# Kernel optimization log

Hardware: AMD Instinct MI355X
Metric: run time of the kernel (lower is better)

Reference implementation:

```python
import jax, jax.numpy as jnp
import numpy as np


def grid_sample_3d(vol, grid):
    """torch F.grid_sample 3D, mode='bilinear' (trilinear), align_corners=True.
    vol:  [B, C, Din, Hin, Win]
    grid: [B, Dout, Hout, Wout, 3] with xyz in [-1, 1] (x->W, y->H, z->D)
    returns [B, C, Dout, Hout, Wout]
    """
    B, C, Din, Hin, Win = vol.shape
    v = jnp.transpose(vol, (0, 2, 3, 4, 1))
    # align_corners=True: -1 -> 0, +1 -> size-1
    ix = (grid[..., 0] + 1.0) * 0.5 * (Win - 1)
    iy = (grid[..., 1] + 1.0) * 0.5 * (Hin - 1)
    iz = (grid[..., 2] + 1.0) * 0.5 * (Din - 1)
    x0 = jnp.floor(ix); y0 = jnp.floor(iy); z0 = jnp.floor(iz)
    wx = (ix - x0)[..., None]
    wy = (iy - y0)[..., None]
    wz = (iz - z0)[..., None]
    x0i = jnp.clip(x0.astype(jnp.int32), 0, Win - 1); x1i = jnp.clip(x0i + 1, 0, Win - 1)
    y0i = jnp.clip(y0.astype(jnp.int32), 0, Hin - 1); y1i = jnp.clip(y0i + 1, 0, Hin - 1)
    z0i = jnp.clip(z0.astype(jnp.int32), 0, Din - 1); z1i = jnp.clip(z0i + 1, 0, Din - 1)
    b = jnp.arange(B)[:, None, None, None]
    g = lambda z, y, x: v[b, z, y, x]  # [B, Dout, Hout, Wout, C]
    # interpolate along x, then y, then z
    c00 = g(z0i, y0i, x0i) * (1.0 - wx) + g(z0i, y0i, x1i) * wx
    c01 = g(z0i, y1i, x0i) * (1.0 - wx) + g(z0i, y1i, x1i) * wx
    c10 = g(z1i, y0i, x0i) * (1.0 - wx) + g(z1i, y0i, x1i) * wx
    c11 = g(z1i, y1i, x0i) * (1.0 - wx) + g(z1i, y1i, x1i) * wx
    c0 = c00 * (1.0 - wy) + c01 * wy
    c1 = c10 * (1.0 - wy) + c11 * wy
    out = c0 * (1.0 - wz) + c1 * wz  # [B, Dout, Hout, Wout, C]
    return jnp.transpose(out, (0, 4, 1, 2, 3))


def setup_inputs() -> dict:
    B, C, G, T = 2, 4, 128, 96
    key = jax.random.key(0)
    k1, k2, k3, k4 = jax.random.split(key, 4)
    grids = jax.random.uniform(k1, (B, G, G, G, 3), jnp.float32, minval=-1.0, maxval=1.0)
    deformation = jax.random.normal(k2, (B, 3, G, G, G), jnp.float32) * 0.1
    correction = jax.random.normal(k3, (B, C, G, G, G), jnp.float32) * 0.05
    template = jax.random.normal(k4, (B, C, T, T, T), jnp.float32)
    return {"grids": grids, "deformation": deformation, "correction": correction, "template": template}


def reference(grids, deformation, correction, template):
    # deformation: [B,3,W,H,D] -> [B,D,H,W,3]
    defp = jnp.transpose(deformation, (0, 4, 3, 2, 1))
    field = jnp.tanh(grids + defp)
    out = grid_sample_3d(template, field)           # [B,C,D,H,W]
    out = jnp.transpose(out, (0, 1, 4, 3, 2)) + correction  # [B,C,W,H,D]
    return (out, defp)
```

## Files before the change

kernel.cpp:

```cpp
#include <hip/hip_runtime.h>
#include <stdint.h>

#define G  128
#define TT 96
#define NB 2
#define NC 4
#define CS (TT * TT * TT)

typedef float f32x4 __attribute__((ext_vector_type(4)));
typedef float f32x2 __attribute__((ext_vector_type(2)));
typedef _Float16 f16x8 __attribute__((ext_vector_type(8)));
typedef _Float16 f16x8u __attribute__((ext_vector_type(8), aligned(8)));

__global__ __launch_bounds__(256) void tmpl_repack_f16(
        const float* __restrict__ tmpl, f16x8* __restrict__ out) {
    const int NP = NB * (CS / 2);
    int idx = blockIdx.x * 256 + threadIdx.x;
    if (idx >= NP) return;
    int b  = idx / (CS / 2);
    int s2 = idx - b * (CS / 2);
    const float* base = tmpl + (size_t)b * NC * CS + (size_t)s2 * 2;
    f16x8 o;
#pragma unroll
    for (int c = 0; c < NC; ++c) {
        f32x2 v = *(const f32x2*)(base + (size_t)c * CS);
        o[c]     = (_Float16)v.x;
        o[4 + c] = (_Float16)v.y;
    }
    out[idx] = o;
}

template <bool PACKED>
__global__ __launch_bounds__(256, 8) void fused_sample_kernel(
        const float* __restrict__ grids,
        const float* __restrict__ deform,
        const float* __restrict__ corr,
        const f16x8* __restrict__ tmpl_f16,
        const float* __restrict__ tmpl_raw,
        float* __restrict__ out2,
        float* __restrict__ defp) {
    __shared__ float lds[3][32][33];

    int blk = blockIdx.x;
    int wt = blk & 3;
    int dt = (blk >> 2) & 3;
    int h  = (blk >> 4) & 127;
    int b  = blk >> 11;
    int w0 = wt << 5, d0 = dt << 5;
    int tid = threadIdx.x;

    for (int idx = tid; idx < 768; idx += 256) {
        int c   = idx >> 8;
        int rem = idx & 255;
        int i   = rem >> 3;
        int j4  = (rem & 7) << 2;
        size_t off = ((((size_t)b * 3 + c) * G + (w0 + i)) * G + h) * G + (d0 + j4);
        f32x4 v = __builtin_nontemporal_load((const f32x4*)(deform + off));
        lds[c][j4 + 0][i] = v.x;
        lds[c][j4 + 1][i] = v.y;
        lds[c][j4 + 2][i] = v.z;
        lds[c][j4 + 3][i] = v.w;
    }
    __syncthreads();

    for (int idx = tid; idx < 768; idx += 256) {
        int j = idx / 24;
        int t = idx - j * 24;
        size_t off = (((((size_t)b * G + (d0 + j)) * G + h) * G + w0) * 3) + (size_t)t * 4;
        f32x4 gv = __builtin_nontemporal_load((const f32x4*)(grids + off));
        float dv[4];
#pragma unroll
        for (int k = 0; k < 4; ++k) {
            int e = t * 4 + k;
            int i = e / 3;
            int c = e - 3 * i;
            float d = lds[c][j][i];
            dv[k] = d;
            lds[c][j][i] = tanhf(gv[k] + d);
        }
        __builtin_nontemporal_store(*(f32x4*)dv, (f32x4*)(defp + off));
    }
    __syncthreads();

    const float SC = 0.5f * (TT - 1);
    const char* tb16 = (const char*)tmpl_f16 + (size_t)b * ((size_t)CS * 8);
    for (int p = tid; p < 1024; p += 256) {
        int i = p >> 5;
        int j = p & 31;
        float ix = (lds[0][j][i] + 1.0f) * SC;
        float iy = (lds[1][j][i] + 1.0f) * SC;
        float iz = (lds[2][j][i] + 1.0f) * SC;
        int x0 = min(max((int)floorf(ix), 0), TT - 2);
        int y0 = min(max((int)floorf(iy), 0), TT - 2);
        int z0 = min(max((int)floorf(iz), 0), TT - 2);
        float wx = ix - (float)x0;
        float wy = iy - (float)y0;
        float wz = iz - (float)z0;
        float mx = 1.0f - wx, my = 1.0f - wy, mz = 1.0f - wz;

        float r0, r1, r2, r3;
        if (PACKED) {
            int y1 = y0 + 1, z1 = z0 + 1;
            int zy00 = (z0 * TT + y0) * TT + x0;
            int zy01 = (z0 * TT + y1) * TT + x0;
            int zy10 = (z1 * TT + y0) * TT + x0;
            int zy11 = (z1 * TT + y1) * TT + x0;
            f16x8 v00 = *(const f16x8u*)(tb16 + (size_t)zy00 * 8);
            f16x8 v01 = *(const f16x8u*)(tb16 + (size_t)zy01 * 8);
            f16x8 v10 = *(const f16x8u*)(tb16 + (size_t)zy10 * 8);
            f16x8 v11 = *(const f16x8u*)(tb16 + (size_t)zy11 * 8);
            float a00 = my * mz, a01 = wy * mz, a10 = my * wz, a11 = wy * wz;
            float r[4];
#pragma unroll
            for (int c = 0; c < NC; ++c) {
                float t00 = (float)v00[c] * mx + (float)v00[4 + c] * wx;
                float t01 = (float)v01[c] * mx + (float)v01[4 + c] * wx;
                float t10 = (float)v10[c] * mx + (float)v10[4 + c] * wx;
                float t11 = (float)v11[c] * mx + (float)v11[4 + c] * wx;
                r[c] = t00 * a00 + t01 * a01 + t10 * a10 + t11 * a11;
            }
            r0 = r[0]; r1 = r[1]; r2 = r[2]; r3 = r[3];
        } else {
            int x1 = x0 + 1, y1 = y0 + 1, z1 = z0 + 1;
            float w000 = mx * my * mz, w001 = wx * my * mz;
            float w010 = mx * wy * mz, w011 = wx * wy * mz;
            float w100 = mx * my * wz, w101 = wx * my * wz;
            float w110 = mx * wy * wz, w111 = wx * wy * wz;
            size_t i000 = ((size_t)z0 * TT + y0) * TT + x0;
            size_t i001 = ((size_t)z0 * TT + y0) * TT + x1;
            size_t i010 = ((size_t)z0 * TT + y1) * TT + x0;
            size_t i011 = ((size_t)z0 * TT + y1) * TT + x1;
            size_t i100 = ((size_t)z1 * TT + y0) * TT + x0;
            size_t i101 = ((size_t)z1 * TT + y0) * TT + x1;
            size_t i110 = ((size_t)z1 * TT + y1) * TT + x0;
            size_t i111 = ((size_t)z1 * TT + y1) * TT + x1;
            float rr[4];
#pragma unroll
            for (int c = 0; c < NC; ++c) {
                const float* tb = tmpl_raw + ((size_t)b * NC + c) * CS;
                rr[c] = tb[i000]*w000 + tb[i001]*w001 + tb[i010]*w010 + tb[i011]*w011
                      + tb[i100]*w100 + tb[i101]*w101 + tb[i110]*w110 + tb[i111]*w111;
            }
            r0 = rr[0]; r1 = rr[1]; r2 = rr[2]; r3 = rr[3];
        }

        int w = w0 + i, d = d0 + j;
        size_t obase = ((((size_t)b * NC) * (size_t)G + w) * G + h) * G + d;
        const size_t cstride = (size_t)G * G * G;
        float c0 = __builtin_nontemporal_load(corr + obase + 0 * cstride);
        float c1 = __builtin_nontemporal_load(corr + obase + 1 * cstride);
        float c2 = __builtin_nontemporal_load(corr + obase + 2 * cstride);
        float c3 = __builtin_nontemporal_load(corr + obase + 3 * cstride);
        __builtin_nontemporal_store(r0 + c0, out2 + obase + 0 * cstride);
        __builtin_nontemporal_store(r1 + c1, out2 + obase + 1 * cstride);
        __builtin_nontemporal_store(r2 + c2, out2 + obase + 2 * cstride);
        __builtin_nontemporal_store(r3 + c3, out2 + obase + 3 * cstride);
    }
}

extern "C" void kernel_launch(void* const* d_in, const int* in_sizes, int n_in,
                              void* d_out, int out_size, void* d_ws, size_t ws_size,
                              hipStream_t stream) {
    const float* grids  = (const float*)d_in[0];
    const float* deform = (const float*)d_in[1];
    const float* corr   = (const float*)d_in[2];
    const float* tmpl   = (const float*)d_in[3];
    float* out2 = (float*)d_out;
    float* defp = out2 + (size_t)NB * NC * G * G * G;
    f16x8* tmpl_f16 = (f16x8*)d_ws;

    const size_t ws_needed = (size_t)NB * CS * 8;
    const bool packed = (ws_size >= ws_needed);

    if (packed) {
        int np = NB * (CS / 2);
        tmpl_repack_f16<<<(np + 255) / 256, 256, 0, stream>>>(tmpl, tmpl_f16);
    }

    int nblk = NB * G * 16;
    if (packed) {
        fused_sample_kernel<true><<<nblk, 256, 0, stream>>>(
            grids, deform, corr, tmpl_f16, tmpl, out2, defp);
    } else {
        fused_sample_kernel<false><<<nblk, 256, 0, stream>>>(
            grids, deform, corr, tmpl_f16, tmpl, out2, defp);
    }
}
```

Measured before the change: 347.2 us.

## Process four d-points per thread with vectorized LDS, corr and output access

```diff
diff --git a/kernel.cpp b/kernel.cpp
--- a/kernel.cpp
+++ b/kernel.cpp
@@ -31,7 +31,7 @@
 }
 
 template <bool PACKED>
-__global__ __launch_bounds__(256, 8) void fused_sample_kernel(
+__global__ __launch_bounds__(256, 4) void fused_sample_kernel(
         const float* __restrict__ grids,
         const float* __restrict__ deform,
         const float* __restrict__ corr,
@@ -39,7 +39,7 @@
         const float* __restrict__ tmpl_raw,
         float* __restrict__ out2,
         float* __restrict__ defp) {
-    __shared__ float lds[3][32][33];
+    __shared__ float lds[3][32][36];
 
     int blk = blockIdx.x;
     int wt = blk & 3;
@@ -56,10 +56,7 @@
         int j4  = (rem & 7) << 2;
         size_t off = ((((size_t)b * 3 + c) * G + (w0 + i)) * G + h) * G + (d0 + j4);
         f32x4 v = __builtin_nontemporal_load((const f32x4*)(deform + off));
-        lds[c][j4 + 0][i] = v.x;
-        lds[c][j4 + 1][i] = v.y;
-        lds[c][j4 + 2][i] = v.z;
-        lds[c][j4 + 3][i] = v.w;
+        *(f32x4*)&lds[c][i][j4] = v;
     }
     __syncthreads();
 
@@ -74,9 +71,9 @@
             int e = t * 4 + k;
             int i = e / 3;
             int c = e - 3 * i;
-            float d = lds[c][j][i];
+            float d = lds[c][i][j];
             dv[k] = d;
-            lds[c][j][i] = tanhf(gv[k] + d);
+            lds[c][i][j] = tanhf(gv[k] + d);
         }
         __builtin_nontemporal_store(*(f32x4*)dv, (f32x4*)(defp + off));
     }
@@ -84,77 +81,92 @@
 
     const float SC = 0.5f * (TT - 1);
     const char* tb16 = (const char*)tmpl_f16 + (size_t)b * ((size_t)CS * 8);
-    for (int p = tid; p < 1024; p += 256) {
-        int i = p >> 5;
-        int j = p & 31;
-        float ix = (lds[0][j][i] + 1.0f) * SC;
-        float iy = (lds[1][j][i] + 1.0f) * SC;
-        float iz = (lds[2][j][i] + 1.0f) * SC;
-        int x0 = min(max((int)floorf(ix), 0), TT - 2);
-        int y0 = min(max((int)floorf(iy), 0), TT - 2);
-        int z0 = min(max((int)floorf(iz), 0), TT - 2);
-        float wx = ix - (float)x0;
-        float wy = iy - (float)y0;
-        float wz = iz - (float)z0;
-        float mx = 1.0f - wx, my = 1.0f - wy, mz = 1.0f - wz;
-
-        float r0, r1, r2, r3;
+    {
+        int i  = tid >> 3;
+        int j4 = (tid & 7) << 2;
+
+        f32x4 fx = *(const f32x4*)&lds[0][i][j4];
+        f32x4 fy = *(const f32x4*)&lds[1][i][j4];
+        f32x4 fz = *(const f32x4*)&lds[2][i][j4];
+
+        float wx[4], wy[4], wz[4];
+        int base[4];
+#pragma unroll
+        for (int k = 0; k < 4; ++k) {
+            float ix = (fx[k] + 1.0f) * SC;
+            float iy = (fy[k] + 1.0f) * SC;
+            float iz = (fz[k] + 1.0f) * SC;
+            int x0 = min(max((int)floorf(ix), 0), TT - 2);
+            int y0 = min(max((int)floorf(iy), 0), TT - 2);
+            int z0 = min(max((int)floorf(iz), 0), TT - 2);
+            wx[k] = ix - (float)x0;
+            wy[k] = iy - (float)y0;
+            wz[k] = iz - (float)z0;
+            base[k] = (z0 * TT + y0) * TT + x0;
+        }
+
+        float r[4][4];
         if (PACKED) {
-            int y1 = y0 + 1, z1 = z0 + 1;
-            int zy00 = (z0 * TT + y0) * TT + x0;
-            int zy01 = (z0 * TT + y1) * TT + x0;
-            int zy10 = (z1 * TT + y0) * TT + x0;
-            int zy11 = (z1 * TT + y1) * TT + x0;
-            f16x8 v00 = *(const f16x8u*)(tb16 + (size_t)zy00 * 8);
-            f16x8 v01 = *(const f16x8u*)(tb16 + (size_t)zy01 * 8);
-            f16x8 v10 = *(const f16x8u*)(tb16 + (size_t)zy10 * 8);
-            f16x8 v11 = *(const f16x8u*)(tb16 + (size_t)zy11 * 8);
-            float a00 = my * mz, a01 = wy * mz, a10 = my * wz, a11 = wy * wz;
-            float r[4];
-#pragma unroll
-            for (int c = 0; c < NC; ++c) {
-                float t00 = (float)v00[c] * mx + (float)v00[4 + c] * wx;
-                float t01 = (float)v01[c] * mx + (float)v01[4 + c] * wx;
-                float t10 = (float)v10[c] * mx + (float)v10[4 + c] * wx;
-                float t11 = (float)v11[c] * mx + (float)v11[4 + c] * wx;
-                r[c] = t00 * a00 + t01 * a01 + t10 * a10 + t11 * a11;
+            f16x8 v00[4], v01[4], v10[4], v11[4];
+#pragma unroll
+            for (int k = 0; k < 4; ++k) {
+                v00[k] = *(const f16x8u*)(tb16 + ((size_t)base[k]) * 8);
+                v01[k] = *(const f16x8u*)(tb16 + ((size_t)(base[k] + TT)) * 8);
+                v10[k] = *(const f16x8u*)(tb16 + ((size_t)(base[k] + TT * TT)) * 8);
+                v11[k] = *(const f16x8u*)(tb16 + ((size_t)(base[k] + TT * TT + TT)) * 8);
             }
-            r0 = r[0]; r1 = r[1]; r2 = r[2]; r3 = r[3];
+#pragma unroll
+            for (int k = 0; k < 4; ++k) {
+                float mx = 1.0f - wx[k], my = 1.0f - wy[k], mz = 1.0f - wz[k];
+                float a00 = my * mz, a01 = wy[k] * mz;
+                float a10 = my * wz[k], a11 = wy[k] * wz[k];
+#pragma unroll
+                for (int c = 0; c < NC; ++c) {
+                    float t00 = (float)v00[k][c] * mx + (float)v00[k][4 + c] * wx[k];
+                    float t01 = (float)v01[k][c] * mx + (float)v01[k][4 + c] * wx[k];
+                    float t10 = (float)v10[k][c] * mx + (float)v10[k][4 + c] * wx[k];
+                    float t11 = (float)v11[k][c] * mx + (float)v11[k][4 + c] * wx[k];
+                    r[k][c] = t00 * a00 + t01 * a01 + t10 * a10 + t11 * a11;
+                }
+            }
         } else {
-            int x1 = x0 + 1, y1 = y0 + 1, z1 = z0 + 1;
-            float w000 = mx * my * mz, w001 = wx * my * mz;
-            float w010 = mx * wy * mz, w011 = wx * wy * mz;
-            float w100 = mx * my * wz, w101 = wx * my * wz;
-            float w110 = mx * wy * wz, w111 = wx * wy * wz;
-            size_t i000 = ((size_t)z0 * TT + y0) * TT + x0;
-            size_t i001 = ((size_t)z0 * TT + y0) * TT + x1;
-            size_t i010 = ((size_t)z0 * TT + y1) * TT + x0;
-            size_t i011 = ((size_t)z0 * TT + y1) * TT + x1;
-            size_t i100 = ((size_t)z1 * TT + y0) * TT + x0;
-            size_t i101 = ((size_t)z1 * TT + y0) * TT + x1;
-            size_t i110 = ((size_t)z1 * TT + y1) * TT + x0;
-            size_t i111 = ((size_t)z1 * TT + y1) * TT + x1;
-            float rr[4];
-#pragma unroll
-            for (int c = 0; c < NC; ++c) {
-                const float* tb = tmpl_raw + ((size_t)b * NC + c) * CS;
-                rr[c] = tb[i000]*w000 + tb[i001]*w001 + tb[i010]*w010 + tb[i011]*w011
-                      + tb[i100]*w100 + tb[i101]*w101 + tb[i110]*w110 + tb[i111]*w111;
+#pragma unroll
+            for (int k = 0; k < 4; ++k) {
+                float mx = 1.0f - wx[k], my = 1.0f - wy[k], mz = 1.0f - wz[k];
+                float w000 = mx * my * mz, w001 = wx[k] * my * mz;
+                float w010 = mx * wy[k] * mz, w011 = wx[k] * wy[k] * mz;
+                float w100 = mx * my * wz[k], w101 = wx[k] * my * wz[k];
+                float w110 = mx * wy[k] * wz[k], w111 = wx[k] * wy[k] * wz[k];
+                size_t i000 = (size_t)base[k];
+                size_t i001 = i000 + 1;
+                size_t i010 = i000 + TT;
+                size_t i011 = i010 + 1;
+                size_t i100 = i000 + TT * TT;
+                size_t i101 = i100 + 1;
+                size_t i110 = i100 + TT;
+                size_t i111 = i110 + 1;
+#pragma unroll
+                for (int c = 0; c < NC; ++c) {
+                    const float* tb = tmpl_raw + ((size_t)b * NC + c) * CS;
+                    r[k][c] = tb[i000]*w000 + tb[i001]*w001 + tb[i010]*w010 + tb[i011]*w011
+                            + tb[i100]*w100 + tb[i101]*w101 + tb[i110]*w110 + tb[i111]*w111;
+                }
             }
-            r0 = rr[0]; r1 = rr[1]; r2 = rr[2]; r3 = rr[3];
-        }
-
-        int w = w0 + i, d = d0 + j;
+        }
+
+        int w = w0 + i, d = d0 + j4;
         size_t obase = ((((size_t)b * NC) * (size_t)G + w) * G + h) * G + d;
         const size_t cstride = (size_t)G * G * G;
-        float c0 = __builtin_nontemporal_load(corr + obase + 0 * cstride);
-        float c1 = __builtin_nontemporal_load(corr + obase + 1 * cstride);
-        float c2 = __builtin_nontemporal_load(corr + obase + 2 * cstride);
-        float c3 = __builtin_nontemporal_load(corr + obase + 3 * cstride);
-        __builtin_nontemporal_store(r0 + c0, out2 + obase + 0 * cstride);
-        __builtin_nontemporal_store(r1 + c1, out2 + obase + 1 * cstride);
-        __builtin_nontemporal_store(r2 + c2, out2 + obase + 2 * cstride);
-        __builtin_nontemporal_store(r3 + c3, out2 + obase + 3 * cstride);
+#pragma unroll
+        for (int c = 0; c < NC; ++c) {
+            f32x4 cv = __builtin_nontemporal_load((const f32x4*)(corr + obase + c * cstride));
+            f32x4 ov;
+            ov.x = r[0][c] + cv.x;
+            ov.y = r[1][c] + cv.y;
+            ov.z = r[2][c] + cv.z;
+            ov.w = r[3][c] + cv.w;
+            __builtin_nontemporal_store(ov, (f32x4*)(out2 + obase + c * cstride));
+        }
     }
 }
 
```

Result: faster. 333.3 us (-4.0%).
